# Performance work log

Measured on AMD Instinct MI355X. Metric: run time of the kernel, lower is better.

The kernel has to match this reference:

```python
import jax, jax.numpy as jnp
import numpy as np

TEMPERATURE = 8.0  # sqrt(d_head=64)


def setup_inputs() -> dict:
    key = jax.random.key(0)
    ks = jax.random.split(key, 6)
    shape = (4, 16, 2048, 64)  # [B, H, L, d_head]
    names = ["q_real", "q_imag", "k_real", "k_imag", "v_real", "v_imag"]
    return {n: jax.random.normal(k, shape, dtype=jnp.float32) for n, k in zip(names, ks)}


def reference(q_real, q_imag, k_real, k_imag, v_real, v_imag):
    # attn = | (q / T) @ conj(k)^H |
    # complex matmul with b = conj(k)^T: br = k_r^T, bi = -k_i^T
    qr = q_real / TEMPERATURE
    qi = q_imag / TEMPERATURE
    # [B,H,Lq,Lk]
    s_real = jnp.einsum("bhqd,bhkd->bhqk", qr, k_real) + jnp.einsum("bhqd,bhkd->bhqk", qi, k_imag)
    s_imag = jnp.einsum("bhqd,bhkd->bhqk", qi, k_real) - jnp.einsum("bhqd,bhkd->bhqk", qr, k_imag)
    attn = jax.nn.softmax(jnp.sqrt(s_real * s_real + s_imag * s_imag), axis=-1)
    # dropout p=0.0 (eval) -> identity
    out_real = jnp.einsum("bhqk,bhkd->bhqd", attn, v_real)
    out_imag = jnp.einsum("bhqk,bhkd->bhqd", attn, v_imag)
    # torch.view_as_complex(stack([real, imag], -1)) -> represent as stacked last dim
    output = jnp.stack([out_real, out_imag], axis=-1)  # [B,H,L,d,2]
    return output, attn
```

## Files before the change

### kernel.cpp

```cpp
#include <hip/hip_runtime.h>
#include <hip/hip_bf16.h>

constexpr int kL  = 2048;
constexpr int kD  = 64;
constexpr int kBH = 64;
constexpr size_t kAttnOff = (size_t)kBH * kL * kD * 2;

typedef __bf16 bf16x8 __attribute__((ext_vector_type(8)));
typedef __bf16 bf16x4 __attribute__((ext_vector_type(4)));
typedef float  f32x4  __attribute__((ext_vector_type(4)));
typedef unsigned int u32x4 __attribute__((ext_vector_type(4)));

static __device__ inline bf16x8 neg8(bf16x8 v) {
  u32x4 t = __builtin_bit_cast(u32x4, v);
  t ^= 0x80008000u;
  return __builtin_bit_cast(bf16x8, t);
}

static __device__ inline bf16x8 pack8(const float4& a, const float4& b) {
  bf16x8 p;
  p[0]=(__bf16)a.x; p[1]=(__bf16)a.y; p[2]=(__bf16)a.z; p[3]=(__bf16)a.w;
  p[4]=(__bf16)b.x; p[5]=(__bf16)b.y; p[6]=(__bf16)b.z; p[7]=(__bf16)b.w;
  return p;
}

static __device__ inline void gl_lds16(char* l, const char* g) {
  __builtin_amdgcn_global_load_lds(
      (const __attribute__((address_space(1))) void*)g,
      (__attribute__((address_space(3))) void*)l, 16, 0, 0);
}

__global__ __launch_bounds__(256) void prep_all_kernel(
    const float* __restrict__ kr_g, const float* __restrict__ ki_g,
    const float* __restrict__ vr_g, const float* __restrict__ vi_g,
    __hip_bfloat16* __restrict__ kb_r, __hip_bfloat16* __restrict__ kb_i,
    __hip_bfloat16* __restrict__ vt_r, __hip_bfloat16* __restrict__ vt_i)
{
  __shared__ __align__(16) char lds_raw[2 * 8192];
  char* tr = lds_raw;
  char* ti = lds_raw + 8192;

  const int tid = threadIdx.x;
  const int bh  = blockIdx.x >> 5;
  const int kb  = blockIdx.x & 31;
  const int k0  = kb * 64;
  const size_t tb = ((size_t)bh * 32 + kb) * 8192;

  const int row = tid >> 2;
  const int d0  = (tid & 3) << 4;
  const size_t gb = ((size_t)bh * kL + k0 + row) * kD + d0;
  const int swz = (row & 7) << 4;

  {
    float4 x0 = *(const float4*)(kr_g + gb);
    float4 x1 = *(const float4*)(kr_g + gb + 4);
    float4 x2 = *(const float4*)(kr_g + gb + 8);
    float4 x3 = *(const float4*)(kr_g + gb + 12);
    *(bf16x8*)((char*)kb_r + tb + row * 128 + ((d0 * 2) ^ swz))      = pack8(x0, x1);
    *(bf16x8*)((char*)kb_r + tb + row * 128 + ((d0 * 2 + 16) ^ swz)) = pack8(x2, x3);
    float4 y0 = *(const float4*)(ki_g + gb);
    float4 y1 = *(const float4*)(ki_g + gb + 4);
    float4 y2 = *(const float4*)(ki_g + gb + 8);
    float4 y3 = *(const float4*)(ki_g + gb + 12);
    *(bf16x8*)((char*)kb_i + tb + row * 128 + ((d0 * 2) ^ swz))      = pack8(y0, y1);
    *(bf16x8*)((char*)kb_i + tb + row * 128 + ((d0 * 2 + 16) ^ swz)) = pack8(y2, y3);
  }

  {
    float4 x0 = *(const float4*)(vr_g + gb);
    float4 x1 = *(const float4*)(vr_g + gb + 4);
    float4 x2 = *(const float4*)(vr_g + gb + 8);
    float4 x3 = *(const float4*)(vr_g + gb + 12);
    *(bf16x8*)(tr + row * 128 + ((d0 * 2) ^ swz))      = pack8(x0, x1);
    *(bf16x8*)(tr + row * 128 + ((d0 * 2 + 16) ^ swz)) = pack8(x2, x3);
    float4 y0 = *(const float4*)(vi_g + gb);
    float4 y1 = *(const float4*)(vi_g + gb + 4);
    float4 y2 = *(const float4*)(vi_g + gb + 8);
    float4 y3 = *(const float4*)(vi_g + gb + 12);
    *(bf16x8*)(ti + row * 128 + ((d0 * 2) ^ swz))      = pack8(y0, y1);
    *(bf16x8*)(ti + row * 128 + ((d0 * 2 + 16) ^ swz)) = pack8(y2, y3);
  }
  __syncthreads();
  {
    const int d  = tid >> 2;
    const int kc = (tid & 3) << 4;
    char* outr = (char*)vt_r + tb + d * 128;
    char* outi = (char*)vt_i + tb + d * 128;
    const int oswz = (d & 7) << 4;
    bf16x8 pr0, pr1, pi0, pi1;
#pragma unroll
    for (int j = 0; j < 8; ++j) {
      const int k1 = kc + j;
      const int k2 = kc + 8 + j;
      const int b1 = k1 * 128 + ((d * 2) ^ ((k1 & 7) << 4));
      const int b2 = k2 * 128 + ((d * 2) ^ ((k2 & 7) << 4));
      pr0[j] = *(const __bf16*)(tr + b1);
      pr1[j] = *(const __bf16*)(tr + b2);
      pi0[j] = *(const __bf16*)(ti + b1);
      pi1[j] = *(const __bf16*)(ti + b2);
    }
    *(bf16x8*)(outr + ((kc * 2) ^ oswz))      = pr0;
    *(bf16x8*)(outr + ((kc * 2 + 16) ^ oswz)) = pr1;
    *(bf16x8*)(outi + ((kc * 2) ^ oswz))      = pi0;
    *(bf16x8*)(outi + ((kc * 2 + 16) ^ oswz)) = pi1;
  }
}

__global__ __launch_bounds__(256) void prep_k_kernel(
    const float* __restrict__ kr_g, const float* __restrict__ ki_g,
    __hip_bfloat16* __restrict__ kb_r, __hip_bfloat16* __restrict__ kb_i)
{
  const int tid = threadIdx.x;
  const int bh  = blockIdx.x >> 5;
  const int kb  = blockIdx.x & 31;
  const int k0  = kb * 64;
  const size_t tb = ((size_t)bh * 32 + kb) * 8192;

  const int row = tid >> 2;
  const int d0  = (tid & 3) << 4;
  const size_t gb = ((size_t)bh * kL + k0 + row) * kD + d0;
  const int swz = (row & 7) << 4;

  float4 x0 = *(const float4*)(kr_g + gb);
  float4 x1 = *(const float4*)(kr_g + gb + 4);
  float4 x2 = *(const float4*)(kr_g + gb + 8);
  float4 x3 = *(const float4*)(kr_g + gb + 12);
  *(bf16x8*)((char*)kb_r + tb + row * 128 + ((d0 * 2) ^ swz))      = pack8(x0, x1);
  *(bf16x8*)((char*)kb_r + tb + row * 128 + ((d0 * 2 + 16) ^ swz)) = pack8(x2, x3);
  float4 y0 = *(const float4*)(ki_g + gb);
  float4 y1 = *(const float4*)(ki_g + gb + 4);
  float4 y2 = *(const float4*)(ki_g + gb + 8);
  float4 y3 = *(const float4*)(ki_g + gb + 12);
  *(bf16x8*)((char*)kb_i + tb + row * 128 + ((d0 * 2) ^ swz))      = pack8(y0, y1);
  *(bf16x8*)((char*)kb_i + tb + row * 128 + ((d0 * 2 + 16) ^ swz)) = pack8(y2, y3);
}

__global__ __launch_bounds__(256) void prep_v_kernel(
    const float* __restrict__ vr_g, const float* __restrict__ vi_g,
    __hip_bfloat16* __restrict__ vt_r, __hip_bfloat16* __restrict__ vt_i)
{
  __shared__ __align__(16) char lds_raw[2 * 8192];
  char* tr = lds_raw;
  char* ti = lds_raw + 8192;

  const int tid = threadIdx.x;
  const int bh  = blockIdx.x >> 5;
  const int kb  = blockIdx.x & 31;
  const int k0  = kb * 64;
  const size_t tb = ((size_t)bh * 32 + kb) * 8192;

  {
    const int row = tid >> 2;
    const int d0  = (tid & 3) << 4;
    const size_t gb = ((size_t)bh * kL + k0 + row) * kD + d0;
    const int swz = (row & 7) << 4;
    float4 x0 = *(const float4*)(vr_g + gb);
    float4 x1 = *(const float4*)(vr_g + gb + 4);
    float4 x2 = *(const float4*)(vr_g + gb + 8);
    float4 x3 = *(const float4*)(vr_g + gb + 12);
    *(bf16x8*)(tr + row * 128 + ((d0 * 2) ^ swz))      = pack8(x0, x1);
    *(bf16x8*)(tr + row * 128 + ((d0 * 2 + 16) ^ swz)) = pack8(x2, x3);
    float4 y0 = *(const float4*)(vi_g + gb);
    float4 y1 = *(const float4*)(vi_g + gb + 4);
    float4 y2 = *(const float4*)(vi_g + gb + 8);
    float4 y3 = *(const float4*)(vi_g + gb + 12);
    *(bf16x8*)(ti + row * 128 + ((d0 * 2) ^ swz))      = pack8(y0, y1);
    *(bf16x8*)(ti + row * 128 + ((d0 * 2 + 16) ^ swz)) = pack8(y2, y3);
  }
  __syncthreads();
  {
    const int d  = tid >> 2;
    const int kc = (tid & 3) << 4;
    char* outr = (char*)vt_r + tb + d * 128;
    char* outi = (char*)vt_i + tb + d * 128;
    const int oswz = (d & 7) << 4;
    bf16x8 pr0, pr1, pi0, pi1;
#pragma unroll
    for (int j = 0; j < 8; ++j) {
      const int k1 = kc + j;
      const int k2 = kc + 8 + j;
      const int b1 = k1 * 128 + ((d * 2) ^ ((k1 & 7) << 4));
      const int b2 = k2 * 128 + ((d * 2) ^ ((k2 & 7) << 4));
      pr0[j] = *(const __bf16*)(tr + b1);
      pr1[j] = *(const __bf16*)(tr + b2);
      pi0[j] = *(const __bf16*)(ti + b1);
      pi1[j] = *(const __bf16*)(ti + b2);
    }
    *(bf16x8*)(outr + ((kc * 2) ^ oswz))      = pr0;
    *(bf16x8*)(outr + ((kc * 2 + 16) ^ oswz)) = pr1;
    *(bf16x8*)(outi + ((kc * 2) ^ oswz))      = pi0;
    *(bf16x8*)(outi + ((kc * 2 + 16) ^ oswz)) = pi1;
  }
}

__global__ __launch_bounds__(256) void qk_ews(
    const float* __restrict__ qr_g, const float* __restrict__ qi_g,
    const __hip_bfloat16* __restrict__ kb_r, const __hip_bfloat16* __restrict__ kb_i,
    __hip_bfloat16* __restrict__ ews, float* __restrict__ rowsum)
{
  __shared__ __align__(16) char lds_raw[49152];
  char* e_l = lds_raw + 32768 + (threadIdx.x >> 6) * 4096;

  const int tid  = threadIdx.x;
  const int wave = tid >> 6;
  const int lane = tid & 63;
  const int g    = lane >> 4;
  const int r    = lane & 15;

  const int bid = blockIdx.x;
  const int nid = (bid & 7) * 128 + (bid >> 3);
  const int bh  = nid >> 4;
  const int q0w = (nid & 15) * 128 + wave * 32;

  bf16x8 aqr[2][2], aqi[2][2], aqrn[2][2];
#pragma unroll
  for (int qt = 0; qt < 2; ++qt) {
    const size_t qbase = ((size_t)bh * kL + q0w + qt * 16 + r) * kD + g * 8;
#pragma unroll
    for (int f = 0; f < 2; ++f) {
      float4 x0 = *(const float4*)(qr_g + qbase + f * 32);
      float4 x1 = *(const float4*)(qr_g + qbase + f * 32 + 4);
      float4 y0 = *(const float4*)(qi_g + qbase + f * 32);
      float4 y1 = *(const float4*)(qi_g + qbase + f * 32 + 4);
      float xr[8] = {x0.x, x0.y, x0.z, x0.w, x1.x, x1.y, x1.z, x1.w};
      float xi[8] = {y0.x, y0.y, y0.z, y0.w, y1.x, y1.y, y1.z, y1.w};
#pragma unroll
      for (int i = 0; i < 8; ++i) {
        aqr[qt][f][i] = (__bf16)(xr[i] * 0.125f);
        aqi[qt][f][i] = (__bf16)(xi[i] * 0.125f);
      }
      aqrn[qt][f] = neg8(aqr[qt][f]);
    }
  }

  float rs[2] = {0.f, 0.f};
  const int off1 = tid * 16;
  const int off2 = off1 + 4096;
  const size_t tbase = (size_t)bh * 32 * 8192;

  auto ISSUE = [&](char* buf, int t) {
    const char* sr = (const char*)kb_r + tbase + (size_t)t * 8192;
    const char* si = (const char*)kb_i + tbase + (size_t)t * 8192;
    gl_lds16(buf + off1, sr + off1);
    gl_lds16(buf + off2, sr + off2);
    gl_lds16(buf + 8192 + off1, si + off1);
    gl_lds16(buf + 8192 + off2, si + off2);
  };

  ISSUE(lds_raw, 0);

#pragma unroll 1
  for (int t = 0; t < 32; ++t) {
    char* cbuf = lds_raw + (t & 1) * 16384;
    char* nbuf = lds_raw + ((t + 1) & 1) * 16384;
    if (t == 0) asm volatile("s_waitcnt vmcnt(0)" ::: "memory");
    else        asm volatile("s_waitcnt vmcnt(4)" ::: "memory");
    __builtin_amdgcn_s_barrier();
    __builtin_amdgcn_sched_barrier(0);
    if (t < 31) ISSUE(nbuf, t + 1);
    __builtin_amdgcn_sched_barrier(0);
    const int k0 = t * 64;

#pragma unroll
    for (int s = 0; s < 4; ++s) {
      const int krow = s * 16 + r;
      const int swz  = (krow & 7) << 4;
      bf16x8 bkr[2], bki[2];
#pragma unroll
      for (int f = 0; f < 2; ++f) {
        const int byte = krow * 128 + (((f * 32 + g * 8) * 2) ^ swz);
        bkr[f] = *(const bf16x8*)(cbuf + byte);
        bki[f] = *(const bf16x8*)(cbuf + 8192 + byte);
      }
#pragma unroll
      for (int qt = 0; qt < 2; ++qt) {
        f32x4 accr = {0.f, 0.f, 0.f, 0.f};
        f32x4 acci = {0.f, 0.f, 0.f, 0.f};
#pragma unroll
        for (int f = 0; f < 2; ++f) {
          accr = __builtin_amdgcn_mfma_f32_16x16x32_bf16(bkr[f], aqr[qt][f],  accr, 0, 0, 0);
          accr = __builtin_amdgcn_mfma_f32_16x16x32_bf16(bki[f], aqi[qt][f],  accr, 0, 0, 0);
          acci = __builtin_amdgcn_mfma_f32_16x16x32_bf16(bkr[f], aqi[qt][f],  acci, 0, 0, 0);
          acci = __builtin_amdgcn_mfma_f32_16x16x32_bf16(bki[f], aqrn[qt][f], acci, 0, 0, 0);
        }
        float e[4];
#pragma unroll
        for (int i = 0; i < 4; ++i)
          e[i] = __expf(sqrtf(accr[i] * accr[i] + acci[i] * acci[i]));
        rs[qt] += (e[0] + e[1]) + (e[2] + e[3]);
        bf16x4 pe;
#pragma unroll
        for (int i = 0; i < 4; ++i) pe[i] = (__bf16)e[i];
        const int row = qt * 16 + r;
        *(bf16x4*)(e_l + row * 128 + (((s * 16 + g * 4) * 2) ^ ((row & 7) << 4))) = pe;
      }
    }

#pragma unroll
    for (int m = 0; m < 4; ++m) {
      const int row  = m * 8 + (lane >> 3);
      const int byte = row * 128 + (((lane & 7) * 16) ^ ((row & 7) << 4));
      bf16x8 v = *(const bf16x8*)(e_l + byte);
      const size_t base = ((size_t)bh * kL + q0w + row) * kL + k0 + (lane & 7) * 8;
      *(bf16x8*)((__bf16*)ews + base) = v;
    }
  }

#pragma unroll
  for (int qt = 0; qt < 2; ++qt) {
    rs[qt] += __shfl_xor(rs[qt], 16, 64);
    rs[qt] += __shfl_xor(rs[qt], 32, 64);
  }
  if (lane < 16) {
#pragma unroll
    for (int qt = 0; qt < 2; ++qt)
      rowsum[(size_t)bh * kL + q0w + qt * 16 + lane] = rs[qt];
  }
}

__global__ __launch_bounds__(256) void pv_norm(
    const __hip_bfloat16* __restrict__ vt_r, const __hip_bfloat16* __restrict__ vt_i,
    const __hip_bfloat16* __restrict__ ews, float* __restrict__ attn,
    const float* __restrict__ rowsum, float* __restrict__ out)
{
  __shared__ __align__(16) char lds_raw[32768];

  const int tid  = threadIdx.x;
  const int wave = tid >> 6;
  const int lane = tid & 63;
  const int g    = lane >> 4;
  const int r    = lane & 15;

  const int bid = blockIdx.x;
  const int nid = (bid & 7) * 128 + (bid >> 3);
  const int bh  = nid >> 4;
  const int q0w = (nid & 15) * 128 + wave * 32;

  float invA[2];
  size_t ebase[2];
#pragma unroll
  for (int qt = 0; qt < 2; ++qt) {
    invA[qt]  = 1.0f / rowsum[(size_t)bh * kL + q0w + qt * 16 + r];
    ebase[qt] = ((size_t)bh * kL + q0w + qt * 16 + r) * kL;
  }

  f32x4 o_r[2][4], o_i[2][4];
#pragma unroll
  for (int qt = 0; qt < 2; ++qt)
#pragma unroll
    for (int dt = 0; dt < 4; ++dt) {
      o_r[qt][dt] = (f32x4){0.f, 0.f, 0.f, 0.f};
      o_i[qt][dt] = (f32x4){0.f, 0.f, 0.f, 0.f};
    }

  const int off1 = tid * 16;
  const int off2 = off1 + 4096;
  const size_t tbase = (size_t)bh * 32 * 8192;
  char* buf0 = lds_raw;
  char* buf1 = lds_raw + 16384;

  auto ISSUE = [&](char* buf, int t) {
    const char* sr = (const char*)vt_r + tbase + (size_t)t * 8192;
    const char* si = (const char*)vt_i + tbase + (size_t)t * 8192;
    gl_lds16(buf + off1, sr + off1);
    gl_lds16(buf + off2, sr + off2);
    gl_lds16(buf + 8192 + off1, si + off1);
    gl_lds16(buf + 8192 + off2, si + off2);
  };

  bf16x8 efA[2][2], efB[2][2];
  auto LOADE = [&](int t, bf16x8 (&ef)[2][2]) {
#pragma unroll
    for (int kh = 0; kh < 2; ++kh)
#pragma unroll
      for (int qt = 0; qt < 2; ++qt)
        ef[kh][qt] = *(const bf16x8*)((const __bf16*)ews + ebase[qt] + t * 64 + kh * 32 + g * 8);
  };

  auto CHUNK = [&](int t, bf16x8 (&ef)[2][2], const char* cbuf) {
    const int k0 = t * 64;
#pragma unroll
    for (int kh = 0; kh < 2; ++kh)
#pragma unroll
      for (int qt = 0; qt < 2; ++qt) {
        const size_t eb = ebase[qt] + k0 + kh * 32 + g * 8;
        bf16x8 v = ef[kh][qt];
        float4 w0, w1;
        w0.x = (float)v[0] * invA[qt]; w0.y = (float)v[1] * invA[qt];
        w0.z = (float)v[2] * invA[qt]; w0.w = (float)v[3] * invA[qt];
        w1.x = (float)v[4] * invA[qt]; w1.y = (float)v[5] * invA[qt];
        w1.z = (float)v[6] * invA[qt]; w1.w = (float)v[7] * invA[qt];
        *(float4*)(attn + eb)     = w0;
        *(float4*)(attn + eb + 4) = w1;
      }
#pragma unroll
    for (int kh = 0; kh < 2; ++kh)
#pragma unroll
      for (int dt = 0; dt < 4; ++dt) {
        const int d = dt * 16 + r;
        const int byte = d * 128 + (((kh * 32 + g * 8) * 2) ^ ((d & 7) << 4));
        bf16x8 bvr = *(const bf16x8*)(cbuf + byte);
        bf16x8 bvi = *(const bf16x8*)(cbuf + 8192 + byte);
#pragma unroll
        for (int qt = 0; qt < 2; ++qt) {
          o_r[qt][dt] = __builtin_amdgcn_mfma_f32_16x16x32_bf16(ef[kh][qt], bvr, o_r[qt][dt], 0, 0, 0);
          o_i[qt][dt] = __builtin_amdgcn_mfma_f32_16x16x32_bf16(ef[kh][qt], bvi, o_i[qt][dt], 0, 0, 0);
        }
      }
  };

  ISSUE(buf0, 0);
  __builtin_amdgcn_sched_barrier(0);
  LOADE(0, efA);

#pragma unroll 1
  for (int t = 0; t < 32; t += 2) {
    if (t == 0) asm volatile("s_waitcnt vmcnt(4)" ::: "memory");
    else        asm volatile("s_waitcnt vmcnt(12)" ::: "memory");
    __builtin_amdgcn_s_barrier();
    __builtin_amdgcn_sched_barrier(0);
    ISSUE(buf1, t + 1);
    __builtin_amdgcn_sched_barrier(0);
    LOADE(t + 1, efB);
    __builtin_amdgcn_sched_barrier(0);
    CHUNK(t, efA, buf0);

    asm volatile("s_waitcnt vmcnt(12)" ::: "memory");
    __builtin_amdgcn_s_barrier();
    __builtin_amdgcn_sched_barrier(0);
    if (t + 2 < 32) {
      ISSUE(buf0, t + 2);
      __builtin_amdgcn_sched_barrier(0);
      LOADE(t + 2, efA);
      __builtin_amdgcn_sched_barrier(0);
    }
    CHUNK(t + 1, efB, buf1);
  }

#pragma unroll
  for (int qt = 0; qt < 2; ++qt)
#pragma unroll
    for (int i = 0; i < 4; ++i) {
      const size_t q = q0w + qt * 16 + g * 4 + i;
      const float iv = 1.0f / rowsum[(size_t)bh * kL + q];
#pragma unroll
      for (int dt = 0; dt < 4; ++dt) {
        const int d = dt * 16 + r;
        float2 val;
        val.x = o_r[qt][dt][i] * iv;
        val.y = o_i[qt][dt][i] * iv;
        *(float2*)(out + (((size_t)bh * kL + q) * kD + d) * 2) = val;
      }
    }
}

__global__ __launch_bounds__(256) void qk_exp_legacy(
    const float* __restrict__ qr_g, const float* __restrict__ qi_g,
    const float* __restrict__ kr_g, const float* __restrict__ ki_g,
    float* __restrict__ attn, float* __restrict__ rowsum)
{
  __shared__ __align__(16) char lds_raw[16384 + 4 * 4096];
  char* kr_l = lds_raw;
  char* ki_l = lds_raw + 8192;
  char* e_l  = lds_raw + 16384 + (threadIdx.x >> 6) * 4096;

  const int tid  = threadIdx.x;
  const int wave = tid >> 6;
  const int lane = tid & 63;
  const int g    = lane >> 4;
  const int r    = lane & 15;

  const int bid = blockIdx.x;
  const int nid = (bid & 7) * 128 + (bid >> 3);
  const int bh  = nid >> 4;
  const int q0w = (nid & 15) * 128 + wave * 32;

  bf16x8 aqr[2][2], aqi[2][2];
#pragma unroll
  for (int qt = 0; qt < 2; ++qt) {
    const size_t qbase = ((size_t)bh * kL + q0w + qt * 16 + r) * kD + g * 8;
#pragma unroll
    for (int f = 0; f < 2; ++f) {
      float4 x0 = *(const float4*)(qr_g + qbase + f * 32);
      float4 x1 = *(const float4*)(qr_g + qbase + f * 32 + 4);
      float4 y0 = *(const float4*)(qi_g + qbase + f * 32);
      float4 y1 = *(const float4*)(qi_g + qbase + f * 32 + 4);
      float xr[8] = {x0.x, x0.y, x0.z, x0.w, x1.x, x1.y, x1.z, x1.w};
      float xi[8] = {y0.x, y0.y, y0.z, y0.w, y1.x, y1.y, y1.z, y1.w};
#pragma unroll
      for (int i = 0; i < 8; ++i) {
        aqr[qt][f][i] = (__bf16)(xr[i] * 0.125f);
        aqi[qt][f][i] = (__bf16)(xi[i] * 0.125f);
      }
    }
  }

  float rs[2] = {0.f, 0.f};

  for (int k0 = 0; k0 < kL; k0 += 64) {
    __syncthreads();
    {
      const int row = tid >> 2;
      const int d0  = (tid & 3) << 4;
      const size_t gb = ((size_t)bh * kL + k0 + row) * kD + d0;
      const int base = row * 128;
      const int swz  = (row & 7) << 4;
      {
        float4 x0 = *(const float4*)(kr_g + gb);
        float4 x1 = *(const float4*)(kr_g + gb + 4);
        float4 x2 = *(const float4*)(kr_g + gb + 8);
        float4 x3 = *(const float4*)(kr_g + gb + 12);
        *(bf16x8*)(kr_l + base + ((d0 * 2) ^ swz))      = pack8(x0, x1);
        *(bf16x8*)(kr_l + base + ((d0 * 2 + 16) ^ swz)) = pack8(x2, x3);
      }
      {
        float4 x0 = *(const float4*)(ki_g + gb);
        float4 x1 = *(const float4*)(ki_g + gb + 4);
        float4 x2 = *(const float4*)(ki_g + gb + 8);
        float4 x3 = *(const float4*)(ki_g + gb + 12);
        *(bf16x8*)(ki_l + base + ((d0 * 2) ^ swz))      = pack8(x0, x1);
        *(bf16x8*)(ki_l + base + ((d0 * 2 + 16) ^ swz)) = pack8(x2, x3);
      }
    }
    __syncthreads();

#pragma unroll
    for (int s = 0; s < 4; ++s) {
      const int krow = s * 16 + r;
      const int swz  = (krow & 7) << 4;
      bf16x8 bkr[2], bki[2], bkin[2];
#pragma unroll
      for (int f = 0; f < 2; ++f) {
        const int byte = krow * 128 + (((f * 32 + g * 8) * 2) ^ swz);
        bkr[f]  = *(const bf16x8*)(kr_l + byte);
        bki[f]  = *(const bf16x8*)(ki_l + byte);
        bkin[f] = neg8(bki[f]);
      }
#pragma unroll
      for (int qt = 0; qt < 2; ++qt) {
        f32x4 accr = {0.f, 0.f, 0.f, 0.f};
        f32x4 acci = {0.f, 0.f, 0.f, 0.f};
#pragma unroll
        for (int f = 0; f < 2; ++f) {
          accr = __builtin_amdgcn_mfma_f32_16x16x32_bf16(bkr[f],  aqr[qt][f], accr, 0, 0, 0);
          accr = __builtin_amdgcn_mfma_f32_16x16x32_bf16(bki[f],  aqi[qt][f], accr, 0, 0, 0);
          acci = __builtin_amdgcn_mfma_f32_16x16x32_bf16(bkr[f],  aqi[qt][f], acci, 0, 0, 0);
          acci = __builtin_amdgcn_mfma_f32_16x16x32_bf16(bkin[f], aqr[qt][f], acci, 0, 0, 0);
        }
        float e[4];
#pragma unroll
        for (int i = 0; i < 4; ++i)
          e[i] = __expf(sqrtf(accr[i] * accr[i] + acci[i] * acci[i]));
        rs[qt] += (e[0] + e[1]) + (e[2] + e[3]);
        bf16x4 pe;
#pragma unroll
        for (int i = 0; i < 4; ++i) pe[i] = (__bf16)e[i];
        const int row = qt * 16 + r;
        *(bf16x4*)(e_l + row * 128 + (((s * 16 + g * 4) * 2) ^ ((row & 7) << 4))) = pe;
      }
    }

#pragma unroll
    for (int m = 0; m < 4; ++m) {
      const int row  = m * 8 + (lane >> 3);
      const int byte = row * 128 + (((lane & 7) * 16) ^ ((row & 7) << 4));
      bf16x8 v = *(const bf16x8*)(e_l + byte);
      const size_t base = ((size_t)bh * kL + q0w + row) * kL + k0 + (lane & 7) * 8;
      float4 w0, w1;
      w0.x=(float)v[0]; w0.y=(float)v[1]; w0.z=(float)v[2]; w0.w=(float)v[3];
      w1.x=(float)v[4]; w1.y=(float)v[5]; w1.z=(float)v[6]; w1.w=(float)v[7];
      *(float4*)(attn + base)     = w0;
      *(float4*)(attn + base + 4) = w1;
    }
  }

#pragma unroll
  for (int qt = 0; qt < 2; ++qt) {
    rs[qt] += __shfl_xor(rs[qt], 16, 64);
    rs[qt] += __shfl_xor(rs[qt], 32, 64);
  }
  if (lane < 16) {
#pragma unroll
    for (int qt = 0; qt < 2; ++qt)
      rowsum[(size_t)bh * kL + q0w + qt * 16 + lane] = rs[qt];
  }
}

__global__ __launch_bounds__(256) void pv_legacy(
    const float* __restrict__ vr_g, const float* __restrict__ vi_g,
    float* __restrict__ attn, const float* __restrict__ rowsum,
    float* __restrict__ out)
{
  __shared__ __align__(16) char lds_raw[2 * 8192];
  char* vr_l = lds_raw;
  char* vi_l = lds_raw + 8192;

  const int tid  = threadIdx.x;
  const int wave = tid >> 6;
  const int lane = tid & 63;
  const int g    = lane >> 4;
  const int r    = lane & 15;

  const int bid = blockIdx.x;
  const int nid = (bid & 7) * 128 + (bid >> 3);
  const int bh  = nid >> 4;
  const int q0w = (nid & 15) * 128 + wave * 32;

  float invA[2];
#pragma unroll
  for (int qt = 0; qt < 2; ++qt)
    invA[qt] = 1.0f / rowsum[(size_t)bh * kL + q0w + qt * 16 + r];

  f32x4 o_r[2][4], o_i[2][4];
#pragma unroll
  for (int qt = 0; qt < 2; ++qt)
#pragma unroll
    for (int dt = 0; dt < 4; ++dt) {
      o_r[qt][dt] = (f32x4){0.f, 0.f, 0.f, 0.f};
      o_i[qt][dt] = (f32x4){0.f, 0.f, 0.f, 0.f};
    }

  for (int k0 = 0; k0 < kL; k0 += 64) {
    __syncthreads();
    {
      const int p  = tid >> 3;
      const int d0 = (tid & 7) << 3;
      const size_t gb0 = ((size_t)bh * kL + k0 + 2 * p) * kD + d0;
      const size_t gb1 = gb0 + kD;
      float4 a0 = *(const float4*)(vr_g + gb0);
      float4 a1 = *(const float4*)(vr_g + gb0 + 4);
      float4 a2 = *(const float4*)(vr_g + gb1);
      float4 a3 = *(const float4*)(vr_g + gb1 + 4);
      float4 b0 = *(const float4*)(vi_g + gb0);
      float4 b1 = *(const float4*)(vi_g + gb0 + 4);
      float4 b2 = *(const float4*)(vi_g + gb1);
      float4 b3 = *(const float4*)(vi_g + gb1 + 4);
      float vr0[8] = {a0.x, a0.y, a0.z, a0.w, a1.x, a1.y, a1.z, a1.w};
      float vr1[8] = {a2.x, a2.y, a2.z, a2.w, a3.x, a3.y, a3.z, a3.w};
      float vi0[8] = {b0.x, b0.y, b0.z, b0.w, b1.x, b1.y, b1.z, b1.w};
      float vi1[8] = {b2.x, b2.y, b2.z, b2.w, b3.x, b3.y, b3.z, b3.w};
#pragma unroll
      for (int j = 0; j < 8; ++j) {
        const int d = d0 + j;
        const int byte = d * 128 + ((p * 4) ^ ((d & 7) << 4));
        __bf16 pa[2] = {(__bf16)vr0[j], (__bf16)vr1[j]};
        __bf16 pb[2] = {(__bf16)vi0[j], (__bf16)vi1[j]};
        *(unsigned int*)(vr_l + byte) = *(unsigned int*)pa;
        *(unsigned int*)(vi_l + byte) = *(unsigned int*)pb;
      }
    }
    __syncthreads();

#pragma unroll
    for (int kh = 0; kh < 2; ++kh) {
      bf16x8 af[2];
#pragma unroll
      for (int qt = 0; qt < 2; ++qt) {
        const size_t q = q0w + qt * 16 + r;
        const size_t eb = ((size_t)bh * kL + q) * kL + k0 + kh * 32 + g * 8;
        float4 e0 = *(const float4*)(attn + eb);
        float4 e1 = *(const float4*)(attn + eb + 4);
        af[qt][0]=(__bf16)e0.x; af[qt][1]=(__bf16)e0.y; af[qt][2]=(__bf16)e0.z; af[qt][3]=(__bf16)e0.w;
        af[qt][4]=(__bf16)e1.x; af[qt][5]=(__bf16)e1.y; af[qt][6]=(__bf16)e1.z; af[qt][7]=(__bf16)e1.w;
        float4 w0 = {e0.x * invA[qt], e0.y * invA[qt], e0.z * invA[qt], e0.w * invA[qt]};
        float4 w1 = {e1.x * invA[qt], e1.y * invA[qt], e1.z * invA[qt], e1.w * invA[qt]};
        *(float4*)(attn + eb)     = w0;
        *(float4*)(attn + eb + 4) = w1;
      }
#pragma unroll
      for (int dt = 0; dt < 4; ++dt) {
        const int d = dt * 16 + r;
        const int byte = d * 128 + (((kh * 32 + g * 8) * 2) ^ ((d & 7) << 4));
        bf16x8 bvr = *(const bf16x8*)(vr_l + byte);
        bf16x8 bvi = *(const bf16x8*)(vi_l + byte);
#pragma unroll
        for (int qt = 0; qt < 2; ++qt) {
          o_r[qt][dt] = __builtin_amdgcn_mfma_f32_16x16x32_bf16(af[qt], bvr, o_r[qt][dt], 0, 0, 0);
          o_i[qt][dt] = __builtin_amdgcn_mfma_f32_16x16x32_bf16(af[qt], bvi, o_i[qt][dt], 0, 0, 0);
        }
      }
    }
  }

#pragma unroll
  for (int qt = 0; qt < 2; ++qt)
#pragma unroll
    for (int i = 0; i < 4; ++i) {
      const size_t q = q0w + qt * 16 + g * 4 + i;
      const float iv = 1.0f / rowsum[(size_t)bh * kL + q];
#pragma unroll
      for (int dt = 0; dt < 4; ++dt) {
        const int d = dt * 16 + r;
        float2 val;
        val.x = o_r[qt][dt][i] * iv;
        val.y = o_i[qt][dt][i] * iv;
        *(float2*)(out + (((size_t)bh * kL + q) * kD + d) * 2) = val;
      }
    }
}

extern "C" void kernel_launch(void* const* d_in, const int* in_sizes, int n_in,
                              void* d_out, int out_size, void* d_ws, size_t ws_size,
                              hipStream_t stream) {
  const float* qr = (const float*)d_in[0];
  const float* qi = (const float*)d_in[1];
  const float* kr = (const float*)d_in[2];
  const float* ki = (const float*)d_in[3];
  const float* vr = (const float*)d_in[4];
  const float* vi = (const float*)d_in[5];
  float* out  = (float*)d_out;
  float* attn = out + kAttnOff;

  const size_t rowsum_bytes = (size_t)kBH * kL * 4;
  const size_t e_bytes      = (size_t)kBH * kL * kL * 2;
  const size_t tile_bytes   = (size_t)kBH * kL * kD * 2;
  float* rowsum = (float*)d_ws;
  __hip_bfloat16* ews = (__hip_bfloat16*)((char*)d_ws + rowsum_bytes);
  char* tiles = (char*)d_ws + rowsum_bytes + e_bytes;
  __hip_bfloat16* t0 = (__hip_bfloat16*)(tiles);
  __hip_bfloat16* t1 = (__hip_bfloat16*)(tiles + tile_bytes);
  __hip_bfloat16* t2 = (__hip_bfloat16*)(tiles + 2 * tile_bytes);
  __hip_bfloat16* t3 = (__hip_bfloat16*)(tiles + 3 * tile_bytes);

  dim3 gridP(kBH * (kL / 64));
  dim3 gridM(kBH * (kL / 128));

  if (ws_size >= rowsum_bytes + e_bytes + 4 * tile_bytes) {
    prep_all_kernel<<<gridP, 256, 0, stream>>>(kr, ki, vr, vi, t0, t1, t2, t3);
    qk_ews<<<gridM, 256, 0, stream>>>(qr, qi, t0, t1, ews, rowsum);
    pv_norm<<<gridM, 256, 0, stream>>>(t2, t3, ews, attn, rowsum, out);
  } else if (ws_size >= rowsum_bytes + e_bytes + 2 * tile_bytes) {
    prep_k_kernel<<<gridP, 256, 0, stream>>>(kr, ki, t0, t1);
    qk_ews<<<gridM, 256, 0, stream>>>(qr, qi, t0, t1, ews, rowsum);
    prep_v_kernel<<<gridP, 256, 0, stream>>>(vr, vi, t0, t1);
    pv_norm<<<gridM, 256, 0, stream>>>(t0, t1, ews, attn, rowsum, out);
  } else {
    qk_exp_legacy<<<gridM, 256, 0, stream>>>(qr, qi, kr, ki, attn, rowsum);
    pv_legacy<<<gridM, 256, 0, stream>>>(vr, vi, attn, rowsum, out);
  }
}
```

Before: 687.5 us.

## Shrink qk_ews LDS staging and simplify pv_norm pipeline to single-step loop

In qk_ews, the loop order is swapped so each 16-row q-tile is written out to ews right after it is computed. This halves the per-wave LDS staging buffer, and the kernel now asks for 4 blocks per CU through launch bounds to raise occupancy. In pv_norm, the hand-unrolled two-stage pipeline that prefetched ews fragments into registers a chunk ahead is replaced by a simple one-chunk-per-iteration loop that loads ews on demand. This should cut register pressure, but the global load latency for ews is no longer hidden by prefetch, and K fragments are reloaded from LDS once per q-tile.

Result: no change. 676.1 us (-1.7%).

```diff
diff --git a/kernel.cpp b/kernel.cpp
--- a/kernel.cpp
+++ b/kernel.cpp
@@ -193,13 +193,13 @@
   }
 }
 
-__global__ __launch_bounds__(256) void qk_ews(
+__global__ __launch_bounds__(256, 4) void qk_ews(
     const float* __restrict__ qr_g, const float* __restrict__ qi_g,
     const __hip_bfloat16* __restrict__ kb_r, const __hip_bfloat16* __restrict__ kb_i,
     __hip_bfloat16* __restrict__ ews, float* __restrict__ rowsum)
 {
-  __shared__ __align__(16) char lds_raw[49152];
-  char* e_l = lds_raw + 32768 + (threadIdx.x >> 6) * 4096;
+  __shared__ __align__(16) char lds_raw[40960];
+  char* e_l = lds_raw + 32768 + (threadIdx.x >> 6) * 2048;
 
   const int tid  = threadIdx.x;
   const int wave = tid >> 6;
@@ -262,18 +262,18 @@
     const int k0 = t * 64;
 
 #pragma unroll
-    for (int s = 0; s < 4; ++s) {
-      const int krow = s * 16 + r;
-      const int swz  = (krow & 7) << 4;
-      bf16x8 bkr[2], bki[2];
-#pragma unroll
-      for (int f = 0; f < 2; ++f) {
-        const int byte = krow * 128 + (((f * 32 + g * 8) * 2) ^ swz);
-        bkr[f] = *(const bf16x8*)(cbuf + byte);
-        bki[f] = *(const bf16x8*)(cbuf + 8192 + byte);
-      }
-#pragma unroll
-      for (int qt = 0; qt < 2; ++qt) {
+    for (int qt = 0; qt < 2; ++qt) {
+#pragma unroll
+      for (int s = 0; s < 4; ++s) {
+        const int krow = s * 16 + r;
+        const int swz  = (krow & 7) << 4;
+        bf16x8 bkr[2], bki[2];
+#pragma unroll
+        for (int f = 0; f < 2; ++f) {
+          const int byte = krow * 128 + (((f * 32 + g * 8) * 2) ^ swz);
+          bkr[f] = *(const bf16x8*)(cbuf + byte);
+          bki[f] = *(const bf16x8*)(cbuf + 8192 + byte);
+        }
         f32x4 accr = {0.f, 0.f, 0.f, 0.f};
         f32x4 acci = {0.f, 0.f, 0.f, 0.f};
 #pragma unroll
@@ -291,18 +291,18 @@
         bf16x4 pe;
 #pragma unroll
         for (int i = 0; i < 4; ++i) pe[i] = (__bf16)e[i];
-        const int row = qt * 16 + r;
-        *(bf16x4*)(e_l + row * 128 + (((s * 16 + g * 4) * 2) ^ ((row & 7) << 4))) = pe;
-      }
-    }
-
-#pragma unroll
-    for (int m = 0; m < 4; ++m) {
-      const int row  = m * 8 + (lane >> 3);
-      const int byte = row * 128 + (((lane & 7) * 16) ^ ((row & 7) << 4));
-      bf16x8 v = *(const bf16x8*)(e_l + byte);
-      const size_t base = ((size_t)bh * kL + q0w + row) * kL + k0 + (lane & 7) * 8;
-      *(bf16x8*)((__bf16*)ews + base) = v;
+        *(bf16x4*)(e_l + r * 128 + (((s * 16 + g * 4) * 2) ^ ((r & 7) << 4))) = pe;
+      }
+      {
+        const int row  = lane >> 2;
+        const int cb   = (lane & 3) * 32;
+        const int swzr = (row & 7) << 4;
+        bf16x8 v0 = *(const bf16x8*)(e_l + row * 128 + (cb ^ swzr));
+        bf16x8 v1 = *(const bf16x8*)(e_l + row * 128 + ((cb + 16) ^ swzr));
+        const size_t base = ((size_t)bh * kL + q0w + qt * 16 + row) * kL + k0 + (lane & 3) * 16;
+        *(bf16x8*)((__bf16*)ews + base)     = v0;
+        *(bf16x8*)((__bf16*)ews + base + 8) = v1;
+      }
     }
   }
 
@@ -356,8 +356,6 @@
   const int off1 = tid * 16;
   const int off2 = off1 + 4096;
   const size_t tbase = (size_t)bh * 32 * 8192;
-  char* buf0 = lds_raw;
-  char* buf1 = lds_raw + 16384;
 
   auto ISSUE = [&](char* buf, int t) {
     const char* sr = (const char*)vt_r + tbase + (size_t)t * 8192;
@@ -368,23 +366,27 @@
     gl_lds16(buf + 8192 + off2, si + off2);
   };
 
-  bf16x8 efA[2][2], efB[2][2];
-  auto LOADE = [&](int t, bf16x8 (&ef)[2][2]) {
-#pragma unroll
-    for (int kh = 0; kh < 2; ++kh)
-#pragma unroll
-      for (int qt = 0; qt < 2; ++qt)
-        ef[kh][qt] = *(const bf16x8*)((const __bf16*)ews + ebase[qt] + t * 64 + kh * 32 + g * 8);
-  };
-
-  auto CHUNK = [&](int t, bf16x8 (&ef)[2][2], const char* cbuf) {
+  ISSUE(lds_raw, 0);
+
+#pragma unroll 1
+  for (int t = 0; t < 32; ++t) {
+    char* cbuf = lds_raw + (t & 1) * 16384;
+    char* nbuf = lds_raw + ((t + 1) & 1) * 16384;
+    if (t == 0) asm volatile("s_waitcnt vmcnt(0)" ::: "memory");
+    else        asm volatile("s_waitcnt vmcnt(8)" ::: "memory");
+    __builtin_amdgcn_s_barrier();
+    __builtin_amdgcn_sched_barrier(0);
+    if (t < 31) ISSUE(nbuf, t + 1);
     const int k0 = t * 64;
+
+    bf16x8 ef[2][2];
 #pragma unroll
     for (int kh = 0; kh < 2; ++kh)
 #pragma unroll
       for (int qt = 0; qt < 2; ++qt) {
         const size_t eb = ebase[qt] + k0 + kh * 32 + g * 8;
-        bf16x8 v = ef[kh][qt];
+        bf16x8 v = *(const bf16x8*)((const __bf16*)ews + eb);
+        ef[kh][qt] = v;
         float4 w0, w1;
         w0.x = (float)v[0] * invA[qt]; w0.y = (float)v[1] * invA[qt];
         w0.z = (float)v[2] * invA[qt]; w0.w = (float)v[3] * invA[qt];
@@ -393,6 +395,7 @@
         *(float4*)(attn + eb)     = w0;
         *(float4*)(attn + eb + 4) = w1;
       }
+
 #pragma unroll
     for (int kh = 0; kh < 2; ++kh)
 #pragma unroll
@@ -407,34 +410,6 @@
           o_i[qt][dt] = __builtin_amdgcn_mfma_f32_16x16x32_bf16(ef[kh][qt], bvi, o_i[qt][dt], 0, 0, 0);
         }
       }
-  };
-
-  ISSUE(buf0, 0);
-  __builtin_amdgcn_sched_barrier(0);
-  LOADE(0, efA);
-
-#pragma unroll 1
-  for (int t = 0; t < 32; t += 2) {
-    if (t == 0) asm volatile("s_waitcnt vmcnt(4)" ::: "memory");
-    else        asm volatile("s_waitcnt vmcnt(12)" ::: "memory");
-    __builtin_amdgcn_s_barrier();
-    __builtin_amdgcn_sched_barrier(0);
-    ISSUE(buf1, t + 1);
-    __builtin_amdgcn_sched_barrier(0);
-    LOADE(t + 1, efB);
-    __builtin_amdgcn_sched_barrier(0);
-    CHUNK(t, efA, buf0);
-
-    asm volatile("s_waitcnt vmcnt(12)" ::: "memory");
-    __builtin_amdgcn_s_barrier();
-    __builtin_amdgcn_sched_barrier(0);
-    if (t + 2 < 32) {
-      ISSUE(buf0, t + 2);
-      __builtin_amdgcn_sched_barrier(0);
-      LOADE(t + 2, efA);
-      __builtin_amdgcn_sched_barrier(0);
-    }
-    CHUNK(t + 1, efB, buf1);
   }
 
 #pragma unroll
```
